# Kernel tuning notes

Hardware: AMD Instinct MI355X
Metric: run time of the kernel (lower is better)

Reference implementation:

```python
import jax, jax.numpy as jnp
import numpy as np

SR = 16000
N_WT = 10
WT_LEN = 512
FIR_TAPS = 31
NU_C = 0.1
N_REFLECT = (FIR_TAPS - 1) // 2
B, L = 16, 160000


def setup_inputs() -> dict:
    key = jax.random.key(0)
    k1, k2, k3, k4 = jax.random.split(key, 4)
    # F0 in a realistic [100, 400) Hz range
    pitch = jax.random.uniform(k1, (B, L, 1), jnp.float32) * 300.0 + 100.0
    envelope = jax.random.uniform(k2, (B, L, 1), jnp.float32)
    # attention weights are 'already softmaxed' over the wavetable axis
    attention = jax.nn.softmax(jax.random.normal(k3, (B, L, N_WT), jnp.float32), axis=-1)
    # learned wavetables, init N(0, 0.01) as in the torch module (n_pure_harmonics=0)
    wavetables = jax.random.normal(k4, (N_WT, WT_LEN), jnp.float32) * 0.01
    # fixed windowed-sinc low-pass FIR (Type I), same construction as __init__
    n = np.arange(-(FIR_TAPS - 1) // 2, 1 + (FIR_TAPS - 1) // 2, dtype=np.float32)
    h = 2.0 * NU_C * np.sinc(2.0 * NU_C * n) * np.hamming(FIR_TAPS)
    fir_h = jnp.asarray(h, jnp.float32)
    return {"pitch": pitch, "envelope": envelope, "attention": attention,
            "wavetables": wavetables, "fir_h": fir_h}


def reference(pitch, envelope, attention, wavetables, fir_h):
    # circular ('reflect' in the repo's naming) pad each wavetable: (W, 512+2*15)
    wt_pad = jnp.concatenate(
        [wavetables[:, -N_REFLECT:], wavetables, wavetables[:, :N_REFLECT]], axis=1)
    # torch conv1d is cross-correlation; jnp.correlate 'valid' matches -> (W, 512)
    wt = jax.vmap(lambda x: jnp.correlate(x, fir_h, mode='valid'))(wt_pad)

    L_wt = WT_LEN
    freqs = pitch[..., 0]                       # (B, L)
    increment = (L_wt / SR) * freqs             # phase increment per sample
    # NOTE: faithful to torch code: increment[0] is the FIRST BATCH ROW (L,)
    index = jnp.cumsum(increment, axis=1) - increment[0]
    index = jnp.remainder(index, L_wt)
    index = jnp.where(L_wt - index < 1e-5, 0.0, index)
    idx_lo_f = jnp.floor(index)
    alpha = index - idx_lo_f                    # (B, L)
    i_lo = idx_lo_f.astype(jnp.int32)
    i_hi = jnp.ceil(index).astype(jnp.int32) % L_wt

    # gather all wavetables at once: (W, B, L)
    lo = jnp.take(wt, i_lo, axis=1)
    hi = jnp.take(wt, i_hi, axis=1)
    wave = lo + alpha[None, :, :] * (hi - lo)   # linear interpolation
    wave = jnp.transpose(wave, (1, 2, 0))       # (B, L, W)

    out = jnp.sum(wave * attention, axis=2, keepdims=True) * envelope  # (B, L, 1)
    return out
```

## Files before the change

### kernel.cpp

```cpp
#include <hip/hip_runtime.h>

#define N_WT_     10
#define WT_LEN_   512
#define FIR_TAPS_ 31
#define N_REFL_   15
#define B_        16
#define L_        160000

constexpr int   TPB   = 256;
constexpr int   NBLK  = L_ / TPB;
constexpr float INCF  = 0.032f;
constexpr int   NG0   = L_ / 16;
constexpr int   NG1   = NG0 / 16;
constexpr int   NG2   = 40;
constexpr int   NG3   = 3;

__global__ void fir_kernel(const float* __restrict__ wavetables,
                           const float* __restrict__ fir_h,
                           float* __restrict__ wt_out) {
    __shared__ float s_pad[WT_LEN_ + 2 * N_REFL_];
    __shared__ float s_h[FIR_TAPS_];
    const int w = blockIdx.x;
    const int i = threadIdx.x;
    if (i < FIR_TAPS_) s_h[i] = fir_h[i];
    for (int j = i; j < WT_LEN_ + 2 * N_REFL_; j += blockDim.x) {
        int src = (j + WT_LEN_ - N_REFL_) % WT_LEN_;
        s_pad[j] = wavetables[w * WT_LEN_ + src];
    }
    __syncthreads();
    float acc = 0.0f;
#pragma unroll
    for (int t = 0; t < FIR_TAPS_; ++t)
        acc = fmaf(s_h[t], s_pad[i + t], acc);
    wt_out[w * WT_LEN_ + i] = acc;
}

__global__ __launch_bounds__(TPB) void ysum_kernel(
        const float* __restrict__ pitch, float* __restrict__ y) {
    __shared__ float s_x[4096];
    const int b = blockIdx.y, bx = blockIdx.x, t = threadIdx.x;
    const float* prow = pitch + (size_t)b * L_;
    const int x0 = bx * 4096;
    for (int i = t; i < 4096; i += TPB) {
        int l = x0 + i;
        s_x[i] = (l < L_) ? INCF * prow[l] : 0.0f;
    }
    __syncthreads();
    const int g = bx * 256 + t;
    if (g < NG0) {
        const float* p = s_x + (g * 16 - x0);
        float acc = 0.0f;
        for (int i = 0; i < 16; ++i) acc += p[i];
        y[b * NG0 + g] = acc;
    }
}

__global__ __launch_bounds__(TPB) void hier_kernel(
        const float* __restrict__ y, float* __restrict__ S1) {
    __shared__ float s_y[NG0];
    __shared__ float s_z[NG1];
    __shared__ float s_w[NG2];
    __shared__ float s_v[NG3];
    __shared__ float s_S4[NG3];
    __shared__ float s_S3[NG2];
    __shared__ float s_S2[NG1];
    const int b = blockIdx.x, t = threadIdx.x;
    const float* yrow = y + (size_t)b * NG0;
    for (int i = t; i < NG0; i += TPB) s_y[i] = yrow[i];
    __syncthreads();
    for (int j = t; j < NG1; j += TPB) {
        float acc = 0.0f;
        for (int i = 0; i < 16; ++i) acc += s_y[16 * j + i];
        s_z[j] = acc;
    }
    __syncthreads();
    if (t < NG2) {
        float acc = 0.0f;
        int hi = min(16 * t + 16, NG1);
        for (int i = 16 * t; i < hi; ++i) acc += s_z[i];
        s_w[t] = acc;
    }
    __syncthreads();
    if (t < NG3) {
        float acc = 0.0f;
        int hi = min(16 * t + 16, NG2);
        for (int i = 16 * t; i < hi; ++i) acc += s_w[i];
        s_v[t] = acc;
    }
    __syncthreads();
    if (t == 0) {
        float run = 0.0f;
        for (int m = 0; m < NG3; ++m) { run += s_v[m]; s_S4[m] = run; }
    }
    __syncthreads();
    if (t < NG2) {
        float acc = 0.0f;
        for (int i = (t >> 4) << 4; i <= t; ++i) acc += s_w[i];
        if (t >= 16) acc = acc + s_S4[(t >> 4) - 1];
        s_S3[t] = acc;
    }
    __syncthreads();
    for (int j = t; j < NG1; j += TPB) {
        float acc = 0.0f;
        for (int i = (j >> 4) << 4; i <= j; ++i) acc += s_z[i];
        if (j >= 16) acc = acc + s_S3[(j >> 4) - 1];
        s_S2[j] = acc;
    }
    __syncthreads();
    float* S1row = S1 + (size_t)b * NG0;
    for (int i = t; i < NG0; i += TPB) {
        float acc = 0.0f;
        for (int q = (i >> 4) << 4; q <= i; ++q) acc += s_y[q];
        if (i >= 16) acc = acc + s_S2[(i >> 4) - 1];
        S1row[i] = acc;
    }
}

__global__ __launch_bounds__(TPB) void synth_kernel(
        const float* __restrict__ pitch,
        const float* __restrict__ envelope,
        const float* __restrict__ attention,
        const float* __restrict__ wt,
        const float* __restrict__ S1,
        float* __restrict__ out) {
    __shared__ float s_wt[N_WT_ * WT_LEN_];
    __shared__ float s_x[TPB];
    const int b = blockIdx.y, c = blockIdx.x, t = threadIdx.x;
    for (int j = t; j < N_WT_ * WT_LEN_; j += TPB) s_wt[j] = wt[j];
    const int l = c * TPB + t;
    const size_t g = (size_t)b * L_ + l;
    s_x[t] = INCF * pitch[g];
    __syncthreads();
    float acc = 0.0f;
    for (int i = t & ~15; i <= t; ++i) acc += s_x[i];
    const int g0 = l >> 4;
    if (g0 > 0) acc = acc + S1[(size_t)b * NG0 + (g0 - 1)];

    float idx = acc - INCF * pitch[l];
    float r = fmodf(idx, 512.0f);
    if (r < 0.0f) r += 512.0f;
    if (512.0f - r < 1e-5f) r = 0.0f;
    float fl = floorf(r);
    float alpha = r - fl;
    int lo = (int)fl;
    int hi = (int)ceilf(r);
    if (hi >= WT_LEN_) hi -= WT_LEN_;

    const float* att = attention + g * N_WT_;
    float a0 = 0.0f;
#pragma unroll
    for (int w = 0; w < N_WT_; ++w) {
        float loV = s_wt[w * WT_LEN_ + lo];
        float hiV = s_wt[w * WT_LEN_ + hi];
        a0 += att[w] * (loV + alpha * (hiV - loV));
    }
    out[g] = a0 * envelope[g];
}

extern "C" void kernel_launch(void* const* d_in, const int* in_sizes, int n_in,
                              void* d_out, int out_size, void* d_ws, size_t ws_size,
                              hipStream_t stream) {
    const float* pitch      = (const float*)d_in[0];
    const float* envelope   = (const float*)d_in[1];
    const float* attention  = (const float*)d_in[2];
    const float* wavetables = (const float*)d_in[3];
    const float* fir_h      = (const float*)d_in[4];
    float*       out        = (float*)d_out;

    char*  ws = (char*)d_ws;
    float* wt = (float*)(ws);
    float* y  = (float*)(ws + 32768);
    float* S1 = (float*)(ws + 32768 + 655360);

    fir_kernel<<<dim3(N_WT_), dim3(WT_LEN_), 0, stream>>>(wavetables, fir_h, wt);
    ysum_kernel<<<dim3(40, B_), dim3(TPB), 0, stream>>>(pitch, y);
    hier_kernel<<<dim3(B_), dim3(TPB), 0, stream>>>(y, S1);
    synth_kernel<<<dim3(NBLK, B_), dim3(TPB), 0, stream>>>(
        pitch, envelope, attention, wt, S1, out);
}
```

Before: 227.2 us.

## Coalesce attention loads via LDS, chunk synth blocks, linearize hierarchical scan

```diff
diff --git a/kernel.cpp b/kernel.cpp
--- a/kernel.cpp
+++ b/kernel.cpp
@@ -8,12 +8,12 @@
 #define L_        160000
 
 constexpr int   TPB   = 256;
-constexpr int   NBLK  = L_ / TPB;
 constexpr float INCF  = 0.032f;
 constexpr int   NG0   = L_ / 16;
 constexpr int   NG1   = NG0 / 16;
 constexpr int   NG2   = 40;
 constexpr int   NG3   = 3;
+constexpr int   CPB   = 5;
 
 __global__ void fir_kernel(const float* __restrict__ wavetables,
                            const float* __restrict__ fir_h,
@@ -55,37 +55,36 @@
     }
 }
 
-__global__ __launch_bounds__(TPB) void hier_kernel(
+__global__ __launch_bounds__(TPB) void scan_kernel(
         const float* __restrict__ y, float* __restrict__ S1) {
     __shared__ float s_y[NG0];
+    __shared__ float s_S1[NG0];
     __shared__ float s_z[NG1];
-    __shared__ float s_w[NG2];
-    __shared__ float s_v[NG3];
-    __shared__ float s_S4[NG3];
-    __shared__ float s_S3[NG2];
     __shared__ float s_S2[NG1];
+    __shared__ float s_w[NG2], s_S3[NG2];
+    __shared__ float s_v[NG3], s_S4[NG3];
     const int b = blockIdx.x, t = threadIdx.x;
     const float* yrow = y + (size_t)b * NG0;
     for (int i = t; i < NG0; i += TPB) s_y[i] = yrow[i];
     __syncthreads();
     for (int j = t; j < NG1; j += TPB) {
-        float acc = 0.0f;
-        for (int i = 0; i < 16; ++i) acc += s_y[16 * j + i];
-        s_z[j] = acc;
+        float a = 0.0f;
+        for (int i = 0; i < 16; ++i) a += s_y[16 * j + i];
+        s_z[j] = a;
     }
     __syncthreads();
     if (t < NG2) {
-        float acc = 0.0f;
+        float a = 0.0f;
         int hi = min(16 * t + 16, NG1);
-        for (int i = 16 * t; i < hi; ++i) acc += s_z[i];
-        s_w[t] = acc;
+        for (int i = 16 * t; i < hi; ++i) a += s_z[i];
+        s_w[t] = a;
     }
     __syncthreads();
     if (t < NG3) {
-        float acc = 0.0f;
+        float a = 0.0f;
         int hi = min(16 * t + 16, NG2);
-        for (int i = 16 * t; i < hi; ++i) acc += s_w[i];
-        s_v[t] = acc;
+        for (int i = 16 * t; i < hi; ++i) a += s_w[i];
+        s_v[t] = a;
     }
     __syncthreads();
     if (t == 0) {
@@ -94,26 +93,33 @@
     }
     __syncthreads();
     if (t < NG2) {
-        float acc = 0.0f;
-        for (int i = (t >> 4) << 4; i <= t; ++i) acc += s_w[i];
-        if (t >= 16) acc = acc + s_S4[(t >> 4) - 1];
-        s_S3[t] = acc;
+        float a = 0.0f;
+        for (int i = (t >> 4) << 4; i <= t; ++i) a += s_w[i];
+        if (t >= 16) a = a + s_S4[(t >> 4) - 1];
+        s_S3[t] = a;
+    }
+    __syncthreads();
+    if (t < NG2) {
+        float r = 0.0f;
+        float carry = (t > 0) ? s_S3[t - 1] : 0.0f;
+        int hi = min(16 * t + 16, NG1);
+        for (int k = 16 * t; k < hi; ++k) {
+            r += s_z[k];
+            s_S2[k] = (t > 0) ? r + carry : r;
+        }
     }
     __syncthreads();
     for (int j = t; j < NG1; j += TPB) {
-        float acc = 0.0f;
-        for (int i = (j >> 4) << 4; i <= j; ++i) acc += s_z[i];
-        if (j >= 16) acc = acc + s_S3[(j >> 4) - 1];
-        s_S2[j] = acc;
+        float r = 0.0f;
+        float carry = (j > 0) ? s_S2[j - 1] : 0.0f;
+        for (int k = 0; k < 16; ++k) {
+            r += s_y[16 * j + k];
+            s_S1[16 * j + k] = (j > 0) ? r + carry : r;
+        }
     }
     __syncthreads();
     float* S1row = S1 + (size_t)b * NG0;
-    for (int i = t; i < NG0; i += TPB) {
-        float acc = 0.0f;
-        for (int q = (i >> 4) << 4; q <= i; ++q) acc += s_y[q];
-        if (i >= 16) acc = acc + s_S2[(i >> 4) - 1];
-        S1row[i] = acc;
-    }
+    for (int i = t; i < NG0; i += TPB) S1row[i] = s_S1[i];
 }
 
 __global__ __launch_bounds__(TPB) void synth_kernel(
@@ -124,37 +130,53 @@
         const float* __restrict__ S1,
         float* __restrict__ out) {
     __shared__ float s_wt[N_WT_ * WT_LEN_];
+    __shared__ float s_att[TPB * N_WT_];
     __shared__ float s_x[TPB];
-    const int b = blockIdx.y, c = blockIdx.x, t = threadIdx.x;
-    for (int j = t; j < N_WT_ * WT_LEN_; j += TPB) s_wt[j] = wt[j];
-    const int l = c * TPB + t;
-    const size_t g = (size_t)b * L_ + l;
-    s_x[t] = INCF * pitch[g];
-    __syncthreads();
-    float acc = 0.0f;
-    for (int i = t & ~15; i <= t; ++i) acc += s_x[i];
-    const int g0 = l >> 4;
-    if (g0 > 0) acc = acc + S1[(size_t)b * NG0 + (g0 - 1)];
-
-    float idx = acc - INCF * pitch[l];
-    float r = fmodf(idx, 512.0f);
-    if (r < 0.0f) r += 512.0f;
-    if (512.0f - r < 1e-5f) r = 0.0f;
-    float fl = floorf(r);
-    float alpha = r - fl;
-    int lo = (int)fl;
-    int hi = (int)ceilf(r);
-    if (hi >= WT_LEN_) hi -= WT_LEN_;
-
-    const float* att = attention + g * N_WT_;
-    float a0 = 0.0f;
+    const int b = blockIdx.y, cb = blockIdx.x, t = threadIdx.x;
+
+    const float4* wt4   = (const float4*)wt;
+    float4*       s_wt4 = (float4*)s_wt;
+    for (int i = t; i < N_WT_ * WT_LEN_ / 4; i += TPB) s_wt4[i] = wt4[i];
+
+    const size_t rowb = (size_t)b * L_;
+
+    for (int cc = 0; cc < CPB; ++cc) {
+        const int    l0 = (cb * CPB + cc) * TPB;
+        const int    l  = l0 + t;
+        const size_t g  = rowb + l;
+        __syncthreads();
+
+        const float4* att4   = (const float4*)(attention + (rowb + l0) * N_WT_);
+        float4*       s_att4 = (float4*)s_att;
+        for (int i = t; i < TPB * N_WT_ / 4; i += TPB) s_att4[i] = att4[i];
+        s_x[t] = INCF * pitch[g];
+        __syncthreads();
+
+        float acc = 0.0f;
+        for (int i = t & ~15; i <= t; ++i) acc += s_x[i];
+        const int g0 = l >> 4;
+        if (g0 > 0) acc = acc + S1[(size_t)b * NG0 + (g0 - 1)];
+
+        float idx = acc - INCF * pitch[l];
+        float r = fmodf(idx, 512.0f);
+        if (r < 0.0f) r += 512.0f;
+        if (512.0f - r < 1e-5f) r = 0.0f;
+        float fl = floorf(r);
+        float alpha = r - fl;
+        int lo = (int)fl;
+        int hi = (int)ceilf(r);
+        if (hi >= WT_LEN_) hi -= WT_LEN_;
+
+        const float* a = s_att + t * N_WT_;
+        float a0 = 0.0f;
 #pragma unroll
-    for (int w = 0; w < N_WT_; ++w) {
-        float loV = s_wt[w * WT_LEN_ + lo];
-        float hiV = s_wt[w * WT_LEN_ + hi];
-        a0 += att[w] * (loV + alpha * (hiV - loV));
-    }
-    out[g] = a0 * envelope[g];
+        for (int w = 0; w < N_WT_; ++w) {
+            float loV = s_wt[w * WT_LEN_ + lo];
+            float hiV = s_wt[w * WT_LEN_ + hi];
+            a0 += a[w] * (loV + alpha * (hiV - loV));
+        }
+        out[g] = a0 * envelope[g];
+    }
 }
 
 extern "C" void kernel_launch(void* const* d_in, const int* in_sizes, int n_in,
@@ -174,7 +196,7 @@
 
     fir_kernel<<<dim3(N_WT_), dim3(WT_LEN_), 0, stream>>>(wavetables, fir_h, wt);
     ysum_kernel<<<dim3(40, B_), dim3(TPB), 0, stream>>>(pitch, y);
-    hier_kernel<<<dim3(B_), dim3(TPB), 0, stream>>>(y, S1);
-    synth_kernel<<<dim3(NBLK, B_), dim3(TPB), 0, stream>>>(
+    scan_kernel<<<dim3(B_), dim3(TPB), 0, stream>>>(y, S1);
+    synth_kernel<<<dim3(L_ / (TPB * CPB), B_), dim3(TPB), 0, stream>>>(
         pitch, envelope, attention, wt, S1, out);
 }
```

Result: faster. 218.0 us (-4.1%).
